# Performance work log

Hardware: AMD Instinct MI355X
Metric: run time of the kernel (lower is better)

## Reference

```python
import jax, jax.numpy as jnp
import numpy as np

WIN = 9
PAD = WIN // 2
LOSS_WEIGHT = 1.0


def _box_sum(x):
    # x: [B,1,H,W]; 9x9 box-filter sum via conv2d with a ones kernel (SAME padding)
    k = jnp.ones((1, 1, WIN, WIN), dtype=x.dtype)
    return jax.lax.conv_general_dilated(
        x, k, window_strides=(1, 1), padding=[(PAD, PAD), (PAD, PAD)],
        dimension_numbers=('NCHW', 'OIHW', 'NCHW'))


def _ncc_map(I, J):
    I2, J2, IJ = I * I, J * J, I * J
    I_sum = _box_sum(I)
    J_sum = _box_sum(J)
    I2_sum = _box_sum(I2)
    J2_sum = _box_sum(J2)
    IJ_sum = _box_sum(IJ)
    n = float(WIN * WIN)
    u_I = I_sum / n
    u_J = J_sum / n
    cross = IJ_sum - u_J * I_sum - u_I * J_sum + u_I * u_J * n
    I_var = I2_sum - 2.0 * u_I * I_sum + u_I * u_I * n
    J_var = J2_sum - 2.0 * u_J * J_sum + u_J * u_J * n
    cc = cross * cross / (I_var * J_var + 1e-5)
    return 1.0 - cc


def setup_inputs() -> dict:
    key = jax.random.key(0)
    k1, k2, k3 = jax.random.split(key, 3)
    shape = (32, 1, 512, 512)
    return {
        'img1': jax.random.uniform(k1, shape, dtype=jnp.float32),
        'img2': jax.random.uniform(k2, shape, dtype=jnp.float32),
        'fusion_img': jax.random.uniform(k3, shape, dtype=jnp.float32),
    }


def reference(img1, img2, fusion_img):
    combined = (_ncc_map(img1, fusion_img) + _ncc_map(img2, fusion_img)) / 2.0
    return jnp.mean(combined) * LOSS_WEIGHT
```

## Files before the change

kernel.cpp:

```cpp
#include <hip/hip_runtime.h>

#define BATCH 32
#define H 512
#define W 512
#define PADR 4
#define WIN 9
#define SEG 16
#define COLS 4
#define NT 128
#define NSTEP (SEG + WIN - 1)
#define SCALE (0.5f / 8388608.0f)

typedef float v4f __attribute__((ext_vector_type(4)));

__global__ __launch_bounds__(NT, 1) void ncc_loss_kernel(
    const float* __restrict__ g1, const float* __restrict__ g2,
    const float* __restrict__ gf, float* __restrict__ out)
{
    const int t  = threadIdx.x;
    const int x0 = t * COLS;
    const int y0 = blockIdx.y * SEG;
    const int b  = blockIdx.z;
    const size_t base = (size_t)b * (size_t)(H * W);
    const int voff = x0 * 4;

    __shared__ __align__(16) float Vl[2][8][520];
    {
        const int gp  = t & 7;
        const int q   = (t >> 3) & 7;
        const int p   = (t >> 6) & 1;
        const int idx = (gp < 4) ? gp : (512 + gp);
        Vl[p][q][idx] = 0.0f;
    }

    v4f buf[2][3];
    auto load_row = [&](int step, int par) {
        const int yr  = y0 - PADR + step;
        const int rec = ((unsigned)yr < (unsigned)H) ? (W * 4) : 0;
        const int yc  = yr < 0 ? 0 : (yr >= H ? H - 1 : yr);
        const size_t roff = base + (size_t)yc * W;
        __amdgpu_buffer_rsrc_t r1 = __builtin_amdgcn_make_buffer_rsrc(
            (void*)(g1 + roff), (short)0, rec, 0x00020000);
        __amdgpu_buffer_rsrc_t r2 = __builtin_amdgcn_make_buffer_rsrc(
            (void*)(g2 + roff), (short)0, rec, 0x00020000);
        __amdgpu_buffer_rsrc_t rf = __builtin_amdgcn_make_buffer_rsrc(
            (void*)(gf + roff), (short)0, rec, 0x00020000);
        buf[par][0] = __builtin_bit_cast(v4f,
            __builtin_amdgcn_raw_buffer_load_b128(r1, voff, 0, 0));
        buf[par][1] = __builtin_bit_cast(v4f,
            __builtin_amdgcn_raw_buffer_load_b128(r2, voff, 0, 0));
        buf[par][2] = __builtin_bit_cast(v4f,
            __builtin_amdgcn_raw_buffer_load_b128(rf, voff, 0, 0));
    };

    float ring[3][WIN][COLS];
#pragma unroll
    for (int im = 0; im < 3; ++im)
#pragma unroll
        for (int i = 0; i < WIN; ++i)
#pragma unroll
            for (int c = 0; c < COLS; ++c) ring[im][i][c] = 0.f;

    float V[8][COLS];
#pragma unroll
    for (int q = 0; q < 8; ++q)
#pragma unroll
        for (int c = 0; c < COLS; ++c) V[q][c] = 0.f;

    float lsum = 0.f;
    const float inv_n = 1.0f / 81.0f;

    load_row(0, 0);

#pragma unroll
    for (int s = 0; s < NSTEP; ++s) {
        if (s + 1 < NSTEP) load_row(s + 1, (s + 1) & 1);

        const v4f A = buf[s & 1][0];
        const v4f C = buf[s & 1][1];
        const v4f F = buf[s & 1][2];
        const int ph = s % WIN;

#pragma unroll
        for (int c = 0; c < COLS; ++c) {
            const float n1 = A[c], n2 = C[c], nf = F[c];
            const float o1 = ring[0][ph][c], o2 = ring[1][ph][c],
                        of = ring[2][ph][c];
            V[0][c] += n1 - o1;
            V[1][c] += n2 - o2;
            V[2][c] += nf - of;
            V[3][c] = fmaf(n1, n1, fmaf(-o1, o1, V[3][c]));
            V[4][c] = fmaf(n2, n2, fmaf(-o2, o2, V[4][c]));
            V[5][c] = fmaf(nf, nf, fmaf(-of, of, V[5][c]));
            V[6][c] = fmaf(n1, nf, fmaf(-o1, of, V[6][c]));
            V[7][c] = fmaf(n2, nf, fmaf(-o2, of, V[7][c]));
            ring[0][ph][c] = n1; ring[1][ph][c] = n2; ring[2][ph][c] = nf;
        }

        if (s >= WIN - 1) {
            const int par = s & 1;
#pragma unroll
            for (int q = 0; q < 8; ++q) {
                v4f v; v.x = V[q][0]; v.y = V[q][1]; v.z = V[q][2]; v.w = V[q][3];
                *(v4f*)&Vl[par][q][4 + x0] = v;
            }
            __syncthreads();
            float S[8][COLS];
#pragma unroll
            for (int q = 0; q < 8; ++q) {
                const v4f w0 = *(const v4f*)&Vl[par][q][x0];
                const v4f w1 = *(const v4f*)&Vl[par][q][x0 + 4];
                const v4f w2 = *(const v4f*)&Vl[par][q][x0 + 8];
                float p = w0.x;  const float a0 = p;
                p += w0.y;       const float a1 = p;
                p += w0.z;       const float a2 = p;
                p += w0.w;
                p += w1.x; p += w1.y; p += w1.z; p += w1.w;
                p += w2.x;       S[q][0] = p;
                p += w2.y;       S[q][1] = p - a0;
                p += w2.z;       S[q][2] = p - a1;
                p += w2.w;       S[q][3] = p - a2;
            }
#pragma unroll
            for (int c = 0; c < COLS; ++c) {
                const float sA = S[0][c], sC = S[1][c], sF = S[2][c];
                const float u1 = sA * inv_n;
                const float u2 = sC * inv_n;
                const float uf = sF * inv_n;
                const float cross1 = fmaf(-sA, uf, S[6][c]);
                const float var1   = fmaf(-sA, u1, S[3][c]);
                const float varf   = fmaf(-sF, uf, S[5][c]);
                const float cross2 = fmaf(-sC, uf, S[7][c]);
                const float var2   = fmaf(-sC, u2, S[4][c]);
                const float d1 = fmaf(var1, varf, 1e-5f);
                const float d2 = fmaf(var2, varf, 1e-5f);
                const float inv = __builtin_amdgcn_rcpf(d1 * d2);
                float num = cross1 * cross1 * d2;
                num = fmaf(cross2 * cross2, d1, num);
                lsum += fmaf(-num, inv, 2.0f);
            }
        }
    }

#pragma unroll
    for (int offd = 32; offd > 0; offd >>= 1)
        lsum += __shfl_down(lsum, offd);
    __shared__ float wsum[2];
    const int lane = t & 63;
    const int wid  = t >> 6;
    if (lane == 0) wsum[wid] = lsum;
    __syncthreads();
    if (t == 0) atomicAdd(out, (wsum[0] + wsum[1]) * SCALE);
}

extern "C" void kernel_launch(void* const* d_in, const int* in_sizes, int n_in,
                              void* d_out, int out_size, void* d_ws, size_t ws_size,
                              hipStream_t stream) {
    const float* img1 = (const float*)d_in[0];
    const float* img2 = (const float*)d_in[1];
    const float* fimg = (const float*)d_in[2];
    float* out = (float*)d_out;

    hipMemsetAsync(out, 0, sizeof(float), stream);

    dim3 grid(1, H / SEG, BATCH);
    ncc_loss_kernel<<<grid, dim3(NT), 0, stream>>>(img1, img2, fimg, out);
}
```

Baseline: 132.1 us.

## Use 2 columns per thread with 256 threads and pair-packed LDS horizontal sums

Each thread now handles two columns instead of four, and the block has 256 threads, which halves per-thread register state. It also permits up to 3 blocks per CU through launch bounds. The shared-memory exchange packs pairs of vertical sums and their prefix into v4f entries, so each thread reads four neighbour entries to form the 9-wide horizontal sums. The double-buffered LDS is replaced by a single buffer guarded by an extra barrier. The intent is higher occupancy to hide memory latency, at the cost of narrower 64-bit loads and more barriers.

```diff
diff --git a/kernel.cpp b/kernel.cpp
--- a/kernel.cpp
+++ b/kernel.cpp
@@ -6,14 +6,15 @@
 #define PADR 4
 #define WIN 9
 #define SEG 16
-#define COLS 4
-#define NT 128
+#define COLS 2
+#define NT 256
 #define NSTEP (SEG + WIN - 1)
 #define SCALE (0.5f / 8388608.0f)
 
+typedef float v2f __attribute__((ext_vector_type(2)));
 typedef float v4f __attribute__((ext_vector_type(4)));
 
-__global__ __launch_bounds__(NT, 1) void ncc_loss_kernel(
+__global__ __launch_bounds__(NT, 3) void ncc_loss_kernel(
     const float* __restrict__ g1, const float* __restrict__ g2,
     const float* __restrict__ gf, float* __restrict__ out)
 {
@@ -24,16 +25,15 @@
     const size_t base = (size_t)b * (size_t)(H * W);
     const int voff = x0 * 4;
 
-    __shared__ __align__(16) float Vl[2][8][520];
-    {
-        const int gp  = t & 7;
-        const int q   = (t >> 3) & 7;
-        const int p   = (t >> 6) & 1;
-        const int idx = (gp < 4) ? gp : (512 + gp);
-        Vl[p][q][idx] = 0.0f;
+    __shared__ v4f Vl[4][260];
+    if (t < 16) {
+        const int qp  = t >> 2;
+        const int g   = t & 3;
+        const int idx = (g < 2) ? g : (256 + g);
+        Vl[qp][idx] = v4f{0.f, 0.f, 0.f, 0.f};
     }
 
-    v4f buf[2][3];
+    v2f buf[2][3];
     auto load_row = [&](int step, int par) {
         const int yr  = y0 - PADR + step;
         const int rec = ((unsigned)yr < (unsigned)H) ? (W * 4) : 0;
@@ -45,12 +45,12 @@
             (void*)(g2 + roff), (short)0, rec, 0x00020000);
         __amdgpu_buffer_rsrc_t rf = __builtin_amdgcn_make_buffer_rsrc(
             (void*)(gf + roff), (short)0, rec, 0x00020000);
-        buf[par][0] = __builtin_bit_cast(v4f,
-            __builtin_amdgcn_raw_buffer_load_b128(r1, voff, 0, 0));
-        buf[par][1] = __builtin_bit_cast(v4f,
-            __builtin_amdgcn_raw_buffer_load_b128(r2, voff, 0, 0));
-        buf[par][2] = __builtin_bit_cast(v4f,
-            __builtin_amdgcn_raw_buffer_load_b128(rf, voff, 0, 0));
+        buf[par][0] = __builtin_bit_cast(v2f,
+            __builtin_amdgcn_raw_buffer_load_b64(r1, voff, 0, 0));
+        buf[par][1] = __builtin_bit_cast(v2f,
+            __builtin_amdgcn_raw_buffer_load_b64(r2, voff, 0, 0));
+        buf[par][2] = __builtin_bit_cast(v2f,
+            __builtin_amdgcn_raw_buffer_load_b64(rf, voff, 0, 0));
     };
 
     float ring[3][WIN][COLS];
@@ -76,9 +76,9 @@
     for (int s = 0; s < NSTEP; ++s) {
         if (s + 1 < NSTEP) load_row(s + 1, (s + 1) & 1);
 
-        const v4f A = buf[s & 1][0];
-        const v4f C = buf[s & 1][1];
-        const v4f F = buf[s & 1][2];
+        const v2f A = buf[s & 1][0];
+        const v2f C = buf[s & 1][1];
+        const v2f F = buf[s & 1][2];
         const int ph = s % WIN;
 
 #pragma unroll
@@ -98,29 +98,41 @@
         }
 
         if (s >= WIN - 1) {
-            const int par = s & 1;
+            if (s > WIN - 1) __syncthreads();
+
+            v4f pk[4];
 #pragma unroll
-            for (int q = 0; q < 8; ++q) {
-                v4f v; v.x = V[q][0]; v.y = V[q][1]; v.z = V[q][2]; v.w = V[q][3];
-                *(v4f*)&Vl[par][q][4 + x0] = v;
+            for (int qp = 0; qp < 4; ++qp) {
+                const int qa = 2 * qp, qb = 2 * qp + 1;
+                v4f v;
+                v.x = V[qa][0]; v.y = V[qa][0] + V[qa][1];
+                v.z = V[qb][0]; v.w = V[qb][0] + V[qb][1];
+                Vl[qp][2 + t] = v;
+                pk[qp] = v;
             }
             __syncthreads();
+
             float S[8][COLS];
 #pragma unroll
-            for (int q = 0; q < 8; ++q) {
-                const v4f w0 = *(const v4f*)&Vl[par][q][x0];
-                const v4f w1 = *(const v4f*)&Vl[par][q][x0 + 4];
-                const v4f w2 = *(const v4f*)&Vl[par][q][x0 + 8];
-                float p = w0.x;  const float a0 = p;
-                p += w0.y;       const float a1 = p;
-                p += w0.z;       const float a2 = p;
-                p += w0.w;
-                p += w1.x; p += w1.y; p += w1.z; p += w1.w;
-                p += w2.x;       S[q][0] = p;
-                p += w2.y;       S[q][1] = p - a0;
-                p += w2.z;       S[q][2] = p - a1;
-                p += w2.w;       S[q][3] = p - a2;
+            for (int qp = 0; qp < 4; ++qp) {
+                const v4f L0 = Vl[qp][t];
+                const v4f L1 = Vl[qp][t + 1];
+                const v4f R1 = Vl[qp][t + 3];
+                const v4f R2 = Vl[qp][t + 4];
+                {
+                    const int q = 2 * qp;
+                    const float com = L1.y + pk[qp].y + R1.y;
+                    S[q][0] = (com + L0.y) + R2.x;
+                    S[q][1] = (com + (L0.y - L0.x)) + R2.y;
+                }
+                {
+                    const int q = 2 * qp + 1;
+                    const float com = L1.w + pk[qp].w + R1.w;
+                    S[q][0] = (com + L0.w) + R2.z;
+                    S[q][1] = (com + (L0.w - L0.z)) + R2.w;
+                }
             }
+
 #pragma unroll
             for (int c = 0; c < COLS; ++c) {
                 const float sA = S[0][c], sC = S[1][c], sF = S[2][c];
@@ -145,12 +157,13 @@
 #pragma unroll
     for (int offd = 32; offd > 0; offd >>= 1)
         lsum += __shfl_down(lsum, offd);
-    __shared__ float wsum[2];
+    __shared__ float wsum[4];
     const int lane = t & 63;
     const int wid  = t >> 6;
     if (lane == 0) wsum[wid] = lsum;
     __syncthreads();
-    if (t == 0) atomicAdd(out, (wsum[0] + wsum[1]) * SCALE);
+    if (t == 0)
+        atomicAdd(out, (wsum[0] + wsum[1] + wsum[2] + wsum[3]) * SCALE);
 }
 
 extern "C" void kernel_launch(void* const* d_in, const int* in_sizes, int n_in,
```

Measured after the change: 127.3 us. -3.7%, faster.

## Use single-wave blocks with DPP lane shifts for horizontal box sum

Applied to the files above, without the earlier changes.

Each block becomes a single 64-thread wave covering a full 512-wide row, with each thread handling 8 columns. The horizontal 9-tap sum now gets neighbour partial sums through DPP row-shift operations instead of an LDS round-trip and a block barrier, and the final two-wave LDS reduction is dropped. This removes the per-row __syncthreads and LDS traffic, at the cost of more registers per thread (larger ring and loads) and half as many waves per block.

```diff
diff --git a/kernel.cpp b/kernel.cpp
--- a/kernel.cpp
+++ b/kernel.cpp
@@ -6,12 +6,49 @@
 #define PADR 4
 #define WIN 9
 #define SEG 16
-#define COLS 4
-#define NT 128
+#define COLS 8
+#define NT 64
 #define NSTEP (SEG + WIN - 1)
 #define SCALE (0.5f / 8388608.0f)
 
 typedef float v4f __attribute__((ext_vector_type(4)));
+
+
+__device__ __forceinline__ float from_left(float v) {
+    return __builtin_bit_cast(float, __builtin_amdgcn_update_dpp(
+        0, __builtin_bit_cast(int, v), 0x138, 0xF, 0xF, true));
+}
+__device__ __forceinline__ float from_right(float v) {
+    return __builtin_bit_cast(float, __builtin_amdgcn_update_dpp(
+        0, __builtin_bit_cast(int, v), 0x130, 0xF, 0xF, true));
+}
+
+#define EMITQ(qi) do {                                        \
+    const float p1 = V[qi][0];                                \
+    const float p2 = p1 + V[qi][1];                           \
+    const float p3 = p2 + V[qi][2];                           \
+    const float p4 = p3 + V[qi][3];                           \
+    const float p5 = p4 + V[qi][4];                           \
+    const float p6 = p5 + V[qi][5];                           \
+    const float p7 = p6 + V[qi][6];                           \
+    const float T  = p7 + V[qi][7];                           \
+    const float l0 = from_left(T - p4);                       \
+    const float l1 = from_left(T - p5);                       \
+    const float l2 = from_left(T - p6);                       \
+    const float l3 = from_left(V[qi][7]);         \
+    const float r4 = from_right(p1);                          \
+    const float r5 = from_right(p2);                          \
+    const float r6 = from_right(p3);                          \
+    const float r7 = from_right(p4);                          \
+    S[qi][0] = l0 + p5;                                       \
+    S[qi][1] = l1 + p6;                                       \
+    S[qi][2] = l2 + p7;                                       \
+    S[qi][3] = l3 + T;                                        \
+    S[qi][4] = T + r4;                                        \
+    S[qi][5] = (T - p1) + r5;                                 \
+    S[qi][6] = (T - p2) + r6;                                 \
+    S[qi][7] = (T - p3) + r7;                                 \
+} while (0)
 
 __global__ __launch_bounds__(NT, 1) void ncc_loss_kernel(
     const float* __restrict__ g1, const float* __restrict__ g2,
@@ -24,16 +61,7 @@
     const size_t base = (size_t)b * (size_t)(H * W);
     const int voff = x0 * 4;
 
-    __shared__ __align__(16) float Vl[2][8][520];
-    {
-        const int gp  = t & 7;
-        const int q   = (t >> 3) & 7;
-        const int p   = (t >> 6) & 1;
-        const int idx = (gp < 4) ? gp : (512 + gp);
-        Vl[p][q][idx] = 0.0f;
-    }
-
-    v4f buf[2][3];
+    v4f buf[2][3][2];
     auto load_row = [&](int step, int par) {
         const int yr  = y0 - PADR + step;
         const int rec = ((unsigned)yr < (unsigned)H) ? (W * 4) : 0;
@@ -45,12 +73,18 @@
             (void*)(g2 + roff), (short)0, rec, 0x00020000);
         __amdgpu_buffer_rsrc_t rf = __builtin_amdgcn_make_buffer_rsrc(
             (void*)(gf + roff), (short)0, rec, 0x00020000);
-        buf[par][0] = __builtin_bit_cast(v4f,
+        buf[par][0][0] = __builtin_bit_cast(v4f,
             __builtin_amdgcn_raw_buffer_load_b128(r1, voff, 0, 0));
-        buf[par][1] = __builtin_bit_cast(v4f,
+        buf[par][0][1] = __builtin_bit_cast(v4f,
+            __builtin_amdgcn_raw_buffer_load_b128(r1, voff + 16, 0, 0));
+        buf[par][1][0] = __builtin_bit_cast(v4f,
             __builtin_amdgcn_raw_buffer_load_b128(r2, voff, 0, 0));
-        buf[par][2] = __builtin_bit_cast(v4f,
+        buf[par][1][1] = __builtin_bit_cast(v4f,
+            __builtin_amdgcn_raw_buffer_load_b128(r2, voff + 16, 0, 0));
+        buf[par][2][0] = __builtin_bit_cast(v4f,
             __builtin_amdgcn_raw_buffer_load_b128(rf, voff, 0, 0));
+        buf[par][2][1] = __builtin_bit_cast(v4f,
+            __builtin_amdgcn_raw_buffer_load_b128(rf, voff + 16, 0, 0));
     };
 
     float ring[3][WIN][COLS];
@@ -76,14 +110,13 @@
     for (int s = 0; s < NSTEP; ++s) {
         if (s + 1 < NSTEP) load_row(s + 1, (s + 1) & 1);
 
-        const v4f A = buf[s & 1][0];
-        const v4f C = buf[s & 1][1];
-        const v4f F = buf[s & 1][2];
         const int ph = s % WIN;
 
 #pragma unroll
         for (int c = 0; c < COLS; ++c) {
-            const float n1 = A[c], n2 = C[c], nf = F[c];
+            const float n1 = buf[s & 1][0][c >> 2][c & 3];
+            const float n2 = buf[s & 1][1][c >> 2][c & 3];
+            const float nf = buf[s & 1][2][c >> 2][c & 3];
             const float o1 = ring[0][ph][c], o2 = ring[1][ph][c],
                         of = ring[2][ph][c];
             V[0][c] += n1 - o1;
@@ -98,29 +131,10 @@
         }
 
         if (s >= WIN - 1) {
-            const int par = s & 1;
-#pragma unroll
-            for (int q = 0; q < 8; ++q) {
-                v4f v; v.x = V[q][0]; v.y = V[q][1]; v.z = V[q][2]; v.w = V[q][3];
-                *(v4f*)&Vl[par][q][4 + x0] = v;
-            }
-            __syncthreads();
             float S[8][COLS];
-#pragma unroll
-            for (int q = 0; q < 8; ++q) {
-                const v4f w0 = *(const v4f*)&Vl[par][q][x0];
-                const v4f w1 = *(const v4f*)&Vl[par][q][x0 + 4];
-                const v4f w2 = *(const v4f*)&Vl[par][q][x0 + 8];
-                float p = w0.x;  const float a0 = p;
-                p += w0.y;       const float a1 = p;
-                p += w0.z;       const float a2 = p;
-                p += w0.w;
-                p += w1.x; p += w1.y; p += w1.z; p += w1.w;
-                p += w2.x;       S[q][0] = p;
-                p += w2.y;       S[q][1] = p - a0;
-                p += w2.z;       S[q][2] = p - a1;
-                p += w2.w;       S[q][3] = p - a2;
-            }
+            EMITQ(0); EMITQ(1); EMITQ(2); EMITQ(3);
+            EMITQ(4); EMITQ(5); EMITQ(6); EMITQ(7);
+
 #pragma unroll
             for (int c = 0; c < COLS; ++c) {
                 const float sA = S[0][c], sC = S[1][c], sF = S[2][c];
@@ -145,12 +159,7 @@
 #pragma unroll
     for (int offd = 32; offd > 0; offd >>= 1)
         lsum += __shfl_down(lsum, offd);
-    __shared__ float wsum[2];
-    const int lane = t & 63;
-    const int wid  = t >> 6;
-    if (lane == 0) wsum[wid] = lsum;
-    __syncthreads();
-    if (t == 0) atomicAdd(out, (wsum[0] + wsum[1]) * SCALE);
+    if (t == 0) atomicAdd(out, lsum * SCALE);
 }
 
 extern "C" void kernel_launch(void* const* d_in, const int* in_sizes, int n_in,
```

Result: no change. 134.6 us (+1.9%).
